# Kernel tuning notes

Hardware: AMD Instinct MI355X
Metric: run time of the kernel (lower is better)

Reference implementation:

```python
import jax, jax.numpy as jnp
import numpy as np

B, N, C = 8, 4096, 768
H = 12
D = C // H  # 64


def setup_inputs() -> dict:
    key = jax.random.key(0)
    k1, k2, k3 = jax.random.split(key, 3)
    x = jax.random.normal(k1, (B, N, C), dtype=jnp.float32)
    Wqkv = jax.random.normal(k2, (C, 3 * C), dtype=jnp.float32) * (C ** -0.5)
    Wproj = jax.random.normal(k3, (C, C), dtype=jnp.float32) * (C ** -0.5)
    bproj = jnp.zeros((C,), dtype=jnp.float32)
    return {"x": x, "Wqkv": Wqkv, "Wproj": Wproj, "bproj": bproj}


def reference(x, Wqkv, Wproj, bproj):
    b, n, c = x.shape
    qkv = x @ Wqkv  # [B,N,3C]
    qkv = qkv.reshape(b, n, 3, H, D).transpose(2, 0, 3, 1, 4)  # [3,B,H,N,D]
    q, k, v = qkv[0], qkv[1], qkv[2]
    # softmax over the sequence axis (dim=-2 in torch => N)
    k = jax.nn.softmax(k, axis=-2)
    # context: [B,H,D,D] -- small d x d intermediate
    context = jnp.einsum('bhnd,bhne->bhde', k, v)
    out = jnp.einsum('bhnd,bhde->bhne', q, context)  # [B,H,N,D]
    out = out.transpose(0, 2, 1, 3).reshape(b, n, c)  # b h n d -> b n (h d)
    return out @ Wproj + bproj
```

## Files before the change

### kernel.cpp

```cpp
#include <hip/hip_runtime.h>
#include <cstdint>
#include <cstddef>


typedef __bf16 bf8_t __attribute__((ext_vector_type(8)));
typedef float f4_t __attribute__((ext_vector_type(4)));

#define DEV_INLINE __device__ __forceinline__

DEV_INLINE void gload16(const void* g, void* l) {
  __builtin_amdgcn_global_load_lds(
      (const __attribute__((address_space(1))) void*)g,
      (__attribute__((address_space(3))) void*)l, 16, 0, 0);
}

__global__ __launch_bounds__(256) void cast_f32_bf16(const float* __restrict__ in,
                                                     __bf16* __restrict__ out, int n4) {
  int i = blockIdx.x * 256 + threadIdx.x;
  if (i >= n4) return;
  float4 f = ((const float4*)in)[i];
  union { __bf16 h[4]; uint2 u; } o;
  o.h[0] = (__bf16)f.x; o.h[1] = (__bf16)f.y; o.h[2] = (__bf16)f.z; o.h[3] = (__bf16)f.w;
  ((uint2*)out)[i] = o.u;
}

__global__ __launch_bounds__(256) void transpose_cast(const float* __restrict__ in,
                                                      __bf16* __restrict__ out, int R, int C) {
  int o = blockIdx.x * 256 + threadIdx.x;
  if (o >= R * C) return;
  int c = o / R, r = o - c * R;
  out[o] = (__bf16)in[r * C + c];
}

__global__ __launch_bounds__(256) void wq_cast(const float* __restrict__ in,
                                               __bf16* __restrict__ out) {
  int o = blockIdx.x * 256 + threadIdx.x;
  int r = o / 768, c = o - r * 768;
  out[o] = (__bf16)in[r * 2304 + c];
}

__global__ __launch_bounds__(256) void gemm1_kv(const __bf16* __restrict__ A,
                                                const __bf16* __restrict__ B,
                                                __bf16* __restrict__ KTo,
                                                __bf16* __restrict__ VTo) {
  constexpr int LDA = 768, LDB = 768, BK = 32, KTOT = 768, NT = 12;
  __shared__ __bf16 sA[128 * 32];
  __shared__ __bf16 sB[128 * 32];
  const int tid = threadIdx.x;
  const int mt = blockIdx.x / NT, nt = blockIdx.x % NT;
  const int lane = tid & 63, wv = tid >> 6;
  const int wr = (wv >> 1) * 64, wc = (wv & 1) * 64;
  const int lr = lane & 15, quad = lane >> 4;

  const int e0 = tid * 8;
  const int srow = e0 >> 5, skk = e0 & 31;
  const __bf16* gA = A + (size_t)(mt * 128 + srow) * LDA + skk;
  const __bf16* gB = B + (size_t)(nt * 128 + srow) * LDB + skk;

  const f4_t fz = {0.f, 0.f, 0.f, 0.f};
  f4_t acc[4][4];
#pragma unroll
  for (int i = 0; i < 4; i++)
#pragma unroll
    for (int j = 0; j < 4; j++) acc[i][j] = fz;

  for (int k0 = 0; k0 < KTOT; k0 += BK) {
    gload16(gA, &sA[e0]);
    gload16(gA + 64 * LDA, &sA[e0 + 2048]);
    gload16(gB, &sB[e0]);
    gload16(gB + 64 * LDB, &sB[e0 + 2048]);
    gA += BK; gB += BK;
    __syncthreads();
    bf8_t af[4], bfm[4];
#pragma unroll
    for (int i = 0; i < 4; i++)
      af[i] = *(const bf8_t*)&sA[(wr + i * 16 + lr) * 32 + quad * 8];
#pragma unroll
    for (int j = 0; j < 4; j++)
      bfm[j] = *(const bf8_t*)&sB[(wc + j * 16 + lr) * 32 + quad * 8];
#pragma unroll
    for (int i = 0; i < 4; i++)
#pragma unroll
      for (int j = 0; j < 4; j++)
        acc[i][j] = __builtin_amdgcn_mfma_f32_16x16x32_bf16(af[i], bfm[j], acc[i][j], 0, 0, 0);
    __syncthreads();
  }

  const int s = nt / 6;
  const int colw0 = (nt % 6) * 128 + wc;
  const int row0 = mt * 128 + wr;
  __bf16* T = (s == 0) ? KTo : VTo;
  const int b = row0 >> 12;
  const int n0 = (row0 & 4095) + quad * 4;
#pragma unroll
  for (int i = 0; i < 4; i++) {
    int n = n0 + i * 16;
#pragma unroll
    for (int j = 0; j < 4; j++) {
      int cw = colw0 + j * 16 + lr;
      int h = cw >> 6, d = cw & 63;
      union { __bf16 h4[4]; uint2 u; } pk;
#pragma unroll
      for (int r = 0; r < 4; r++) pk.h4[r] = (__bf16)acc[i][j][r];
      *(uint2*)&T[((size_t)(b * 12 + h) * 64 + d) * 4096 + n] = pk.u;
    }
  }
}

__global__ __launch_bounds__(256) void softmax_rows(__bf16* __restrict__ KT) {
  __shared__ float red[8];
  __bf16* p = KT + (size_t)blockIdx.x * 4096;
  const int tid = threadIdx.x, lane = tid & 63, wv = tid >> 6;
  bf8_t x0 = *(const bf8_t*)&p[tid * 16];
  bf8_t x1 = *(const bf8_t*)&p[tid * 16 + 8];
  float v[16];
#pragma unroll
  for (int k = 0; k < 8; k++) { v[k] = (float)x0[k]; v[8 + k] = (float)x1[k]; }
  float m = v[0];
#pragma unroll
  for (int k = 1; k < 16; k++) m = fmaxf(m, v[k]);
  for (int o = 32; o; o >>= 1) m = fmaxf(m, __shfl_xor(m, o, 64));
  if (lane == 0) red[wv] = m;
  __syncthreads();
  m = fmaxf(fmaxf(red[0], red[1]), fmaxf(red[2], red[3]));
  float s = 0.f;
#pragma unroll
  for (int k = 0; k < 16; k++) { v[k] = __expf(v[k] - m); s += v[k]; }
  for (int o = 32; o; o >>= 1) s += __shfl_xor(s, o, 64);
  if (lane == 0) red[4 + wv] = s;
  __syncthreads();
  s = red[4] + red[5] + red[6] + red[7];
  float inv = 1.0f / s;
  bf8_t o0, o1;
#pragma unroll
  for (int k = 0; k < 8; k++) { o0[k] = (__bf16)(v[k] * inv); o1[k] = (__bf16)(v[8 + k] * inv); }
  *(bf8_t*)&p[tid * 16] = o0;
  *(bf8_t*)&p[tid * 16 + 8] = o1;
}

__global__ __launch_bounds__(256) void ctx_kernel(const __bf16* __restrict__ KT,
                                                  const __bf16* __restrict__ VT,
                                                  float* __restrict__ part) {
  const int bh = blockIdx.x >> 3, kc = blockIdx.x & 7;
  const int tid = threadIdx.x, lane = tid & 63, wv = tid >> 6;
  const int wr = (wv >> 1) * 32, wc = (wv & 1) * 32;
  const int lr = lane & 15, quad = lane >> 4;
  const __bf16* Ab = KT + (size_t)bh * 64 * 4096;
  const __bf16* Bb = VT + (size_t)bh * 64 * 4096;
  const f4_t fz = {0.f, 0.f, 0.f, 0.f};
  f4_t acc[2][2] = {{fz, fz}, {fz, fz}};
  const int kbeg = kc * 512;
  for (int k0 = kbeg; k0 < kbeg + 512; k0 += 32) {
    bf8_t a[2], b[2];
#pragma unroll
    for (int i = 0; i < 2; i++)
      a[i] = *(const bf8_t*)&Ab[(size_t)(wr + i * 16 + lr) * 4096 + k0 + quad * 8];
#pragma unroll
    for (int j = 0; j < 2; j++)
      b[j] = *(const bf8_t*)&Bb[(size_t)(wc + j * 16 + lr) * 4096 + k0 + quad * 8];
#pragma unroll
    for (int i = 0; i < 2; i++)
#pragma unroll
      for (int j = 0; j < 2; j++)
        acc[i][j] = __builtin_amdgcn_mfma_f32_16x16x32_bf16(a[i], b[j], acc[i][j], 0, 0, 0);
  }
  float* po = part + (size_t)blockIdx.x * 4096;
#pragma unroll
  for (int i = 0; i < 2; i++)
#pragma unroll
    for (int j = 0; j < 2; j++)
#pragma unroll
      for (int r = 0; r < 4; r++)
        po[(wr + i * 16 + quad * 4 + r) * 64 + wc + j * 16 + lr] = acc[i][j][r];
}

__global__ __launch_bounds__(256) void wfused_kernel(const float* __restrict__ part,
                                                     const __bf16* __restrict__ WpT,
                                                     __bf16* __restrict__ B2T) {
  __shared__ __bf16 sctx[64 * 64];
  const int bh = blockIdx.x, cblk = blockIdx.y;
  const int b = bh / 12, h = bh % 12;
  const int tid = threadIdx.x;
  for (int i = tid; i < 4096; i += 256) {
    float s = 0.f;
#pragma unroll
    for (int kc = 0; kc < 8; kc++) s += part[(size_t)(bh * 8 + kc) * 4096 + i];
    sctx[i] = (__bf16)s;
  }
  __syncthreads();
  const int lane = tid & 63, wv = tid >> 6, lr = lane & 15, quad = lane >> 4;
  const int c0 = cblk * 192 + wv * 48;
  const f4_t fz = {0.f, 0.f, 0.f, 0.f};
  f4_t acc[3][4];
#pragma unroll
  for (int i = 0; i < 3; i++)
#pragma unroll
    for (int j = 0; j < 4; j++) acc[i][j] = fz;
#pragma unroll
  for (int k0 = 0; k0 < 64; k0 += 32) {
    bf8_t a[3], bq[4];
#pragma unroll
    for (int i = 0; i < 3; i++)
      a[i] = *(const bf8_t*)&WpT[(size_t)(c0 + i * 16 + lr) * 768 + h * 64 + k0 + quad * 8];
#pragma unroll
    for (int j = 0; j < 4; j++)
      bq[j] = *(const bf8_t*)&sctx[(j * 16 + lr) * 64 + k0 + quad * 8];
#pragma unroll
    for (int i = 0; i < 3; i++)
#pragma unroll
      for (int j = 0; j < 4; j++)
        acc[i][j] = __builtin_amdgcn_mfma_f32_16x16x32_bf16(a[i], bq[j], acc[i][j], 0, 0, 0);
  }
#pragma unroll
  for (int i = 0; i < 3; i++)
#pragma unroll
    for (int j = 0; j < 4; j++)
#pragma unroll
      for (int r = 0; r < 4; r++) {
        int c = c0 + i * 16 + quad * 4 + r;
        int d = j * 16 + lr;
        B2T[((size_t)b * 768 + c) * 768 + h * 64 + d] = (__bf16)acc[i][j][r];
      }
}

__global__ __launch_bounds__(256) void combine_kernel(const __bf16* __restrict__ B2Tall,
                                                      const __bf16* __restrict__ Wq,
                                                      __bf16* __restrict__ Wcomb) {
  constexpr int LD = 768, BK = 32, KTOT = 768;
  __shared__ __bf16 sA[64 * 32];
  __shared__ __bf16 sB[64 * 32];
  const int b = blockIdx.x / 144, rem = blockIdx.x % 144;
  const int mt = rem / 12, nt = rem % 12;
  const __bf16* A = B2Tall + (size_t)b * 768 * 768;
  const int tid = threadIdx.x, lane = tid & 63, wv = tid >> 6;
  const int wr = (wv >> 1) * 32, wc = (wv & 1) * 32;
  const int lr = lane & 15, quad = lane >> 4;

  const int e0 = tid * 8;
  const int srow = e0 >> 5, skk = e0 & 31;
  const __bf16* gA = A + (size_t)(mt * 64 + srow) * LD + skk;
  const __bf16* gB = Wq + (size_t)(nt * 64 + srow) * LD + skk;

  const f4_t fz = {0.f, 0.f, 0.f, 0.f};
  f4_t acc[2][2] = {{fz, fz}, {fz, fz}};

  for (int k0 = 0; k0 < KTOT; k0 += BK) {
    gload16(gA, &sA[e0]);
    gload16(gB, &sB[e0]);
    gA += BK; gB += BK;
    __syncthreads();
    bf8_t a[2], bq[2];
#pragma unroll
    for (int i = 0; i < 2; i++)
      a[i] = *(const bf8_t*)&sA[(wr + i * 16 + lr) * 32 + quad * 8];
#pragma unroll
    for (int j = 0; j < 2; j++)
      bq[j] = *(const bf8_t*)&sB[(wc + j * 16 + lr) * 32 + quad * 8];
#pragma unroll
    for (int i = 0; i < 2; i++)
#pragma unroll
      for (int j = 0; j < 2; j++)
        acc[i][j] = __builtin_amdgcn_mfma_f32_16x16x32_bf16(a[i], bq[j], acc[i][j], 0, 0, 0);
    __syncthreads();
  }
  __bf16* C = Wcomb + (size_t)b * 768 * 768;
  const int row0 = mt * 64 + wr, col0 = nt * 64 + wc;
#pragma unroll
  for (int i = 0; i < 2; i++)
#pragma unroll
    for (int j = 0; j < 2; j++)
#pragma unroll
      for (int r = 0; r < 4; r++)
        C[(size_t)(row0 + i * 16 + quad * 4 + r) * 768 + col0 + j * 16 + lr] =
            (__bf16)acc[i][j][r];
}

__global__ __launch_bounds__(256) void gemm2_out(const __bf16* __restrict__ A,
                                                 const __bf16* __restrict__ Ball,
                                                 float* __restrict__ C,
                                                 const float* __restrict__ bias) {
  constexpr int LDA = 768, LDB = 768, BK = 32, KTOT = 768, NT = 6;
  __shared__ __bf16 sA[128 * 32];
  __shared__ __bf16 sB[128 * 32];
  const int tid = threadIdx.x;
  const int mt = blockIdx.x / NT, nt = blockIdx.x % NT;
  const __bf16* B = Ball + (size_t)(mt >> 5) * 768 * 768;
  const int lane = tid & 63, wv = tid >> 6;
  const int wr = (wv >> 1) * 64, wc = (wv & 1) * 64;
  const int lr = lane & 15, quad = lane >> 4;

  const int e0 = tid * 8;
  const int srow = e0 >> 5, skk = e0 & 31;
  const __bf16* gA = A + (size_t)(mt * 128 + srow) * LDA + skk;
  const __bf16* gB = B + (size_t)(nt * 128 + srow) * LDB + skk;

  const f4_t fz = {0.f, 0.f, 0.f, 0.f};
  f4_t acc[4][4];
#pragma unroll
  for (int i = 0; i < 4; i++)
#pragma unroll
    for (int j = 0; j < 4; j++) acc[i][j] = fz;

  for (int k0 = 0; k0 < KTOT; k0 += BK) {
    gload16(gA, &sA[e0]);
    gload16(gA + 64 * LDA, &sA[e0 + 2048]);
    gload16(gB, &sB[e0]);
    gload16(gB + 64 * LDB, &sB[e0 + 2048]);
    gA += BK; gB += BK;
    __syncthreads();
    bf8_t af[4], bfm[4];
#pragma unroll
    for (int i = 0; i < 4; i++)
      af[i] = *(const bf8_t*)&sA[(wr + i * 16 + lr) * 32 + quad * 8];
#pragma unroll
    for (int j = 0; j < 4; j++)
      bfm[j] = *(const bf8_t*)&sB[(wc + j * 16 + lr) * 32 + quad * 8];
#pragma unroll
    for (int i = 0; i < 4; i++)
#pragma unroll
      for (int j = 0; j < 4; j++)
        acc[i][j] = __builtin_amdgcn_mfma_f32_16x16x32_bf16(af[i], bfm[j], acc[i][j], 0, 0, 0);
    __syncthreads();
  }

  const int row0 = mt * 128 + wr;
  const int col0 = nt * 128 + wc;
#pragma unroll
  for (int j = 0; j < 4; j++) {
    int col = col0 + j * 16 + lr;
    float bv = bias[col];
#pragma unroll
    for (int i = 0; i < 4; i++)
#pragma unroll
      for (int r = 0; r < 4; r++)
        C[(size_t)(row0 + i * 16 + quad * 4 + r) * 768 + col] = acc[i][j][r] + bv;
  }
}

extern "C" void kernel_launch(void* const* d_in, const int* in_sizes, int n_in,
                              void* d_out, int out_size, void* d_ws, size_t ws_size,
                              hipStream_t stream) {
  const float* x = (const float*)d_in[0];
  const float* Wqkv = (const float*)d_in[1];
  const float* Wproj = (const float*)d_in[2];
  const float* bproj = (const float*)d_in[3];
  float* out = (float*)d_out;

  char* ws = (char*)d_ws;
  __bf16* Xb    = (__bf16*)(ws + 0);
  __bf16* KT    = (__bf16*)(ws + 50331648);
  __bf16* VT    = (__bf16*)(ws + 100663296);
  __bf16* WqkvT = (__bf16*)(ws + 150994944);
  __bf16* Wqc   = (__bf16*)(ws + 154533888);
  __bf16* WpT   = (__bf16*)(ws + 155713536);
  float*  part  = (float*)(ws + 156893184);
  __bf16* B2T   = (__bf16*)(ws + 169476096);
  __bf16* Wcomb = (__bf16*)(ws + 178913280);

  cast_f32_bf16<<<24576, 256, 0, stream>>>(x, Xb, 25165824 / 4);
  transpose_cast<<<(768 * 2304) / 256, 256, 0, stream>>>(Wqkv, WqkvT, 768, 2304);
  wq_cast<<<(768 * 768) / 256, 256, 0, stream>>>(Wqkv, Wqc);
  transpose_cast<<<(768 * 768) / 256, 256, 0, stream>>>(Wproj, WpT, 768, 768);
  gemm1_kv<<<256 * 12, 256, 0, stream>>>(Xb, WqkvT + 768 * 768, KT, VT);
  softmax_rows<<<6144, 256, 0, stream>>>(KT);
  ctx_kernel<<<96 * 8, 256, 0, stream>>>(KT, VT, part);
  wfused_kernel<<<dim3(96, 4), 256, 0, stream>>>(part, WpT, B2T);
  combine_kernel<<<1152, 256, 0, stream>>>(B2T, Wqc, Wcomb);
  gemm2_out<<<256 * 6, 256, 0, stream>>>(Xb, Wcomb, out, bproj);
}
```

Before: 450.6 us.

## Use 32x32 MFMA with swizzled LDS, fold softmax into ctx, tile transposes

```diff
diff --git a/kernel.cpp b/kernel.cpp
--- a/kernel.cpp
+++ b/kernel.cpp
@@ -5,6 +5,7 @@
 
 typedef __bf16 bf8_t __attribute__((ext_vector_type(8)));
 typedef float f4_t __attribute__((ext_vector_type(4)));
+typedef float f16_t __attribute__((ext_vector_type(16)));
 
 #define DEV_INLINE __device__ __forceinline__
 
@@ -26,10 +27,22 @@
 
 __global__ __launch_bounds__(256) void transpose_cast(const float* __restrict__ in,
                                                       __bf16* __restrict__ out, int R, int C) {
-  int o = blockIdx.x * 256 + threadIdx.x;
-  if (o >= R * C) return;
-  int c = o / R, r = o - c * R;
-  out[o] = (__bf16)in[r * C + c];
+  __shared__ float t[64][65];
+  const int tilesR = R >> 6;
+  const int tr = blockIdx.x % tilesR, tc = blockIdx.x / tilesR;
+  const int tx = threadIdx.x & 63, ty = threadIdx.x >> 6;
+  const int r0 = tr * 64, c0 = tc * 64;
+#pragma unroll
+  for (int p = 0; p < 16; p++) {
+    int r = p * 4 + ty;
+    t[r][tx] = in[(size_t)(r0 + r) * C + c0 + tx];
+  }
+  __syncthreads();
+#pragma unroll
+  for (int p = 0; p < 16; p++) {
+    int c = p * 4 + ty;
+    out[(size_t)(c0 + c) * R + r0 + tx] = (__bf16)t[tx][c];
+  }
 }
 
 __global__ __launch_bounds__(256) void wq_cast(const float* __restrict__ in,
@@ -43,73 +56,91 @@
                                                 const __bf16* __restrict__ B,
                                                 __bf16* __restrict__ KTo,
                                                 __bf16* __restrict__ VTo) {
-  constexpr int LDA = 768, LDB = 768, BK = 32, KTOT = 768, NT = 12;
+  constexpr int LDA = 768, LDB = 768, KTOT = 768;
   __shared__ __bf16 sA[128 * 32];
   __shared__ __bf16 sB[128 * 32];
   const int tid = threadIdx.x;
-  const int mt = blockIdx.x / NT, nt = blockIdx.x % NT;
+  const int xcd = blockIdx.x & 7, g = blockIdx.x >> 3;
+  const int mt = xcd * 32 + g / 12, nt = g % 12;
   const int lane = tid & 63, wv = tid >> 6;
   const int wr = (wv >> 1) * 64, wc = (wv & 1) * 64;
-  const int lr = lane & 15, quad = lane >> 4;
-
-  const int e0 = tid * 8;
-  const int srow = e0 >> 5, skk = e0 & 31;
-  const __bf16* gA = A + (size_t)(mt * 128 + srow) * LDA + skk;
-  const __bf16* gB = B + (size_t)(nt * 128 + srow) * LDB + skk;
-
-  const f4_t fz = {0.f, 0.f, 0.f, 0.f};
-  f4_t acc[4][4];
-#pragma unroll
-  for (int i = 0; i < 4; i++)
-#pragma unroll
-    for (int j = 0; j < 4; j++) acc[i][j] = fz;
-
-  for (int k0 = 0; k0 < KTOT; k0 += BK) {
-    gload16(gA, &sA[e0]);
-    gload16(gA + 64 * LDA, &sA[e0 + 2048]);
-    gload16(gB, &sB[e0]);
-    gload16(gB + 64 * LDB, &sB[e0 + 2048]);
-    gA += BK; gB += BK;
-    __syncthreads();
-    bf8_t af[4], bfm[4];
-#pragma unroll
-    for (int i = 0; i < 4; i++)
-      af[i] = *(const bf8_t*)&sA[(wr + i * 16 + lr) * 32 + quad * 8];
-#pragma unroll
-    for (int j = 0; j < 4; j++)
-      bfm[j] = *(const bf8_t*)&sB[(wc + j * 16 + lr) * 32 + quad * 8];
-#pragma unroll
-    for (int i = 0; i < 4; i++)
-#pragma unroll
-      for (int j = 0; j < 4; j++)
-        acc[i][j] = __builtin_amdgcn_mfma_f32_16x16x32_bf16(af[i], bfm[j], acc[i][j], 0, 0, 0);
+  const int l31 = lane & 31, l5 = lane >> 5;
+
+  const int srow = tid >> 2;
+  const int sk = ((tid & 3) ^ ((srow >> 1) & 3)) * 8;
+  const __bf16* gA = A + (size_t)(mt * 128 + srow) * LDA + sk;
+  const __bf16* gB = B + (size_t)(nt * 128 + srow) * LDB + sk;
+
+  const int arow = wr + l31, brow = wc + l31;
+  const int asw = (arow >> 1) & 3, bsw = (brow >> 1) & 3;
+  const int aoff  = arow * 32 + ((l5 ^ asw) * 8);
+  const int aoff2 = arow * 32 + (((2 | l5) ^ asw) * 8);
+  const int boff  = brow * 32 + ((l5 ^ bsw) * 8);
+  const int boff2 = brow * 32 + (((2 | l5) ^ bsw) * 8);
+
+  f16_t acc[2][2];
+#pragma unroll
+  for (int i = 0; i < 2; i++)
+#pragma unroll
+    for (int j = 0; j < 2; j++)
+#pragma unroll
+      for (int e = 0; e < 16; e++) acc[i][j][e] = 0.f;
+
+  for (int k0 = 0; k0 < KTOT; k0 += 32) {
+    gload16(gA, &sA[tid * 8]);
+    gload16(gA + 64 * LDA, &sA[tid * 8 + 2048]);
+    gload16(gB, &sB[tid * 8]);
+    gload16(gB + 64 * LDB, &sB[tid * 8 + 2048]);
+    gA += 32; gB += 32;
+    __syncthreads();
+    bf8_t a0 = *(const bf8_t*)&sA[aoff];
+    bf8_t a1 = *(const bf8_t*)&sA[aoff + 1024];
+    bf8_t b0 = *(const bf8_t*)&sB[boff];
+    bf8_t b1 = *(const bf8_t*)&sB[boff + 1024];
+    acc[0][0] = __builtin_amdgcn_mfma_f32_32x32x16_bf16(a0, b0, acc[0][0], 0, 0, 0);
+    acc[0][1] = __builtin_amdgcn_mfma_f32_32x32x16_bf16(a0, b1, acc[0][1], 0, 0, 0);
+    acc[1][0] = __builtin_amdgcn_mfma_f32_32x32x16_bf16(a1, b0, acc[1][0], 0, 0, 0);
+    acc[1][1] = __builtin_amdgcn_mfma_f32_32x32x16_bf16(a1, b1, acc[1][1], 0, 0, 0);
+    a0 = *(const bf8_t*)&sA[aoff2];
+    a1 = *(const bf8_t*)&sA[aoff2 + 1024];
+    b0 = *(const bf8_t*)&sB[boff2];
+    b1 = *(const bf8_t*)&sB[boff2 + 1024];
+    acc[0][0] = __builtin_amdgcn_mfma_f32_32x32x16_bf16(a0, b0, acc[0][0], 0, 0, 0);
+    acc[0][1] = __builtin_amdgcn_mfma_f32_32x32x16_bf16(a0, b1, acc[0][1], 0, 0, 0);
+    acc[1][0] = __builtin_amdgcn_mfma_f32_32x32x16_bf16(a1, b0, acc[1][0], 0, 0, 0);
+    acc[1][1] = __builtin_amdgcn_mfma_f32_32x32x16_bf16(a1, b1, acc[1][1], 0, 0, 0);
     __syncthreads();
   }
 
   const int s = nt / 6;
+  __bf16* T = (s == 0) ? KTo : VTo;
+  const int row0 = mt * 128 + wr;
+  const int bidx = row0 >> 12;
+  const int n0 = (row0 & 4095) + 4 * l5;
   const int colw0 = (nt % 6) * 128 + wc;
-  const int row0 = mt * 128 + wr;
-  __bf16* T = (s == 0) ? KTo : VTo;
-  const int b = row0 >> 12;
-  const int n0 = (row0 & 4095) + quad * 4;
-#pragma unroll
-  for (int i = 0; i < 4; i++) {
-    int n = n0 + i * 16;
-#pragma unroll
-    for (int j = 0; j < 4; j++) {
-      int cw = colw0 + j * 16 + lr;
-      int h = cw >> 6, d = cw & 63;
-      union { __bf16 h4[4]; uint2 u; } pk;
-#pragma unroll
-      for (int r = 0; r < 4; r++) pk.h4[r] = (__bf16)acc[i][j][r];
-      *(uint2*)&T[((size_t)(b * 12 + h) * 64 + d) * 4096 + n] = pk.u;
+#pragma unroll
+  for (int j = 0; j < 2; j++) {
+    int cw = colw0 + j * 32 + l31;
+    int h = cw >> 6, d = cw & 63;
+    __bf16* Tp = &T[((size_t)(bidx * 12 + h) * 64 + d) * 4096];
+#pragma unroll
+    for (int i = 0; i < 2; i++) {
+      int nb = n0 + i * 32;
+#pragma unroll
+      for (int r2 = 0; r2 < 4; r2++) {
+        union { __bf16 h4[4]; uint2 u; } pk;
+#pragma unroll
+        for (int r = 0; r < 4; r++) pk.h4[r] = (__bf16)acc[i][j][r2 * 4 + r];
+        *(uint2*)&Tp[nb + 8 * r2] = pk.u;
+      }
     }
   }
 }
 
-__global__ __launch_bounds__(256) void softmax_rows(__bf16* __restrict__ KT) {
+__global__ __launch_bounds__(256) void stats_rows(const __bf16* __restrict__ KT,
+                                                  float2* __restrict__ stats) {
   __shared__ float red[8];
-  __bf16* p = KT + (size_t)blockIdx.x * 4096;
+  const __bf16* p = KT + (size_t)blockIdx.x * 4096;
   const int tid = threadIdx.x, lane = tid & 63, wv = tid >> 6;
   bf8_t x0 = *(const bf8_t*)&p[tid * 16];
   bf8_t x1 = *(const bf8_t*)&p[tid * 16 + 8];
@@ -125,21 +156,19 @@
   m = fmaxf(fmaxf(red[0], red[1]), fmaxf(red[2], red[3]));
   float s = 0.f;
 #pragma unroll
-  for (int k = 0; k < 16; k++) { v[k] = __expf(v[k] - m); s += v[k]; }
+  for (int k = 0; k < 16; k++) s += __expf(v[k] - m);
   for (int o = 32; o; o >>= 1) s += __shfl_xor(s, o, 64);
   if (lane == 0) red[4 + wv] = s;
   __syncthreads();
-  s = red[4] + red[5] + red[6] + red[7];
-  float inv = 1.0f / s;
-  bf8_t o0, o1;
-#pragma unroll
-  for (int k = 0; k < 8; k++) { o0[k] = (__bf16)(v[k] * inv); o1[k] = (__bf16)(v[8 + k] * inv); }
-  *(bf8_t*)&p[tid * 16] = o0;
-  *(bf8_t*)&p[tid * 16 + 8] = o1;
+  if (tid == 0) {
+    float st = red[4] + red[5] + red[6] + red[7];
+    stats[blockIdx.x] = make_float2(m, 1.0f / st);
+  }
 }
 
 __global__ __launch_bounds__(256) void ctx_kernel(const __bf16* __restrict__ KT,
                                                   const __bf16* __restrict__ VT,
+                                                  const float2* __restrict__ stats,
                                                   float* __restrict__ part) {
   const int bh = blockIdx.x >> 3, kc = blockIdx.x & 7;
   const int tid = threadIdx.x, lane = tid & 63, wv = tid >> 6;
@@ -147,14 +176,21 @@
   const int lr = lane & 15, quad = lane >> 4;
   const __bf16* Ab = KT + (size_t)bh * 64 * 4096;
   const __bf16* Bb = VT + (size_t)bh * 64 * 4096;
+  float2 st[2];
+  st[0] = stats[bh * 64 + wr + lr];
+  st[1] = stats[bh * 64 + wr + 16 + lr];
   const f4_t fz = {0.f, 0.f, 0.f, 0.f};
   f4_t acc[2][2] = {{fz, fz}, {fz, fz}};
   const int kbeg = kc * 512;
   for (int k0 = kbeg; k0 < kbeg + 512; k0 += 32) {
     bf8_t a[2], b[2];
 #pragma unroll
-    for (int i = 0; i < 2; i++)
-      a[i] = *(const bf8_t*)&Ab[(size_t)(wr + i * 16 + lr) * 4096 + k0 + quad * 8];
+    for (int i = 0; i < 2; i++) {
+      bf8_t raw = *(const bf8_t*)&Ab[(size_t)(wr + i * 16 + lr) * 4096 + k0 + quad * 8];
+#pragma unroll
+      for (int e = 0; e < 8; e++)
+        a[i][e] = (__bf16)(__expf((float)raw[e] - st[i].x) * st[i].y);
+    }
 #pragma unroll
     for (int j = 0; j < 2; j++)
       b[j] = *(const bf8_t*)&Bb[(size_t)(wc + j * 16 + lr) * 4096 + k0 + quad * 8];
@@ -279,61 +315,78 @@
                                                  const __bf16* __restrict__ Ball,
                                                  float* __restrict__ C,
                                                  const float* __restrict__ bias) {
-  constexpr int LDA = 768, LDB = 768, BK = 32, KTOT = 768, NT = 6;
+  constexpr int LDA = 768, LDB = 768, KTOT = 768;
   __shared__ __bf16 sA[128 * 32];
   __shared__ __bf16 sB[128 * 32];
   const int tid = threadIdx.x;
-  const int mt = blockIdx.x / NT, nt = blockIdx.x % NT;
+  const int xcd = blockIdx.x & 7, g = blockIdx.x >> 3;
+  const int mt = xcd * 32 + g / 6, nt = g % 6;
   const __bf16* B = Ball + (size_t)(mt >> 5) * 768 * 768;
   const int lane = tid & 63, wv = tid >> 6;
   const int wr = (wv >> 1) * 64, wc = (wv & 1) * 64;
-  const int lr = lane & 15, quad = lane >> 4;
-
-  const int e0 = tid * 8;
-  const int srow = e0 >> 5, skk = e0 & 31;
-  const __bf16* gA = A + (size_t)(mt * 128 + srow) * LDA + skk;
-  const __bf16* gB = B + (size_t)(nt * 128 + srow) * LDB + skk;
-
-  const f4_t fz = {0.f, 0.f, 0.f, 0.f};
-  f4_t acc[4][4];
-#pragma unroll
-  for (int i = 0; i < 4; i++)
-#pragma unroll
-    for (int j = 0; j < 4; j++) acc[i][j] = fz;
-
-  for (int k0 = 0; k0 < KTOT; k0 += BK) {
-    gload16(gA, &sA[e0]);
-    gload16(gA + 64 * LDA, &sA[e0 + 2048]);
-    gload16(gB, &sB[e0]);
-    gload16(gB + 64 * LDB, &sB[e0 + 2048]);
-    gA += BK; gB += BK;
-    __syncthreads();
-    bf8_t af[4], bfm[4];
-#pragma unroll
-    for (int i = 0; i < 4; i++)
-      af[i] = *(const bf8_t*)&sA[(wr + i * 16 + lr) * 32 + quad * 8];
-#pragma unroll
-    for (int j = 0; j < 4; j++)
-      bfm[j] = *(const bf8_t*)&sB[(wc + j * 16 + lr) * 32 + quad * 8];
-#pragma unroll
-    for (int i = 0; i < 4; i++)
-#pragma unroll
-      for (int j = 0; j < 4; j++)
-        acc[i][j] = __builtin_amdgcn_mfma_f32_16x16x32_bf16(af[i], bfm[j], acc[i][j], 0, 0, 0);
-    __syncthreads();
-  }
-
-  const int row0 = mt * 128 + wr;
+  const int l31 = lane & 31, l5 = lane >> 5;
+
+  const int srow = tid >> 2;
+  const int sk = ((tid & 3) ^ ((srow >> 1) & 3)) * 8;
+  const __bf16* gA = A + (size_t)(mt * 128 + srow) * LDA + sk;
+  const __bf16* gB = B + (size_t)(nt * 128 + srow) * LDB + sk;
+
+  const int arow = wr + l31, brow = wc + l31;
+  const int asw = (arow >> 1) & 3, bsw = (brow >> 1) & 3;
+  const int aoff  = arow * 32 + ((l5 ^ asw) * 8);
+  const int aoff2 = arow * 32 + (((2 | l5) ^ asw) * 8);
+  const int boff  = brow * 32 + ((l5 ^ bsw) * 8);
+  const int boff2 = brow * 32 + (((2 | l5) ^ bsw) * 8);
+
+  f16_t acc[2][2];
+#pragma unroll
+  for (int i = 0; i < 2; i++)
+#pragma unroll
+    for (int j = 0; j < 2; j++)
+#pragma unroll
+      for (int e = 0; e < 16; e++) acc[i][j][e] = 0.f;
+
+  for (int k0 = 0; k0 < KTOT; k0 += 32) {
+    gload16(gA, &sA[tid * 8]);
+    gload16(gA + 64 * LDA, &sA[tid * 8 + 2048]);
+    gload16(gB, &sB[tid * 8]);
+    gload16(gB + 64 * LDB, &sB[tid * 8 + 2048]);
+    gA += 32; gB += 32;
+    __syncthreads();
+    bf8_t a0 = *(const bf8_t*)&sA[aoff];
+    bf8_t a1 = *(const bf8_t*)&sA[aoff + 1024];
+    bf8_t b0 = *(const bf8_t*)&sB[boff];
+    bf8_t b1 = *(const bf8_t*)&sB[boff + 1024];
+    acc[0][0] = __builtin_amdgcn_mfma_f32_32x32x16_bf16(a0, b0, acc[0][0], 0, 0, 0);
+    acc[0][1] = __builtin_amdgcn_mfma_f32_32x32x16_bf16(a0, b1, acc[0][1], 0, 0, 0);
+    acc[1][0] = __builtin_amdgcn_mfma_f32_32x32x16_bf16(a1, b0, acc[1][0], 0, 0, 0);
+    acc[1][1] = __builtin_amdgcn_mfma_f32_32x32x16_bf16(a1, b1, acc[1][1], 0, 0, 0);
+    a0 = *(const bf8_t*)&sA[aoff2];
+    a1 = *(const bf8_t*)&sA[aoff2 + 1024];
+    b0 = *(const bf8_t*)&sB[boff2];
+    b1 = *(const bf8_t*)&sB[boff2 + 1024];
+    acc[0][0] = __builtin_amdgcn_mfma_f32_32x32x16_bf16(a0, b0, acc[0][0], 0, 0, 0);
+    acc[0][1] = __builtin_amdgcn_mfma_f32_32x32x16_bf16(a0, b1, acc[0][1], 0, 0, 0);
+    acc[1][0] = __builtin_amdgcn_mfma_f32_32x32x16_bf16(a1, b0, acc[1][0], 0, 0, 0);
+    acc[1][1] = __builtin_amdgcn_mfma_f32_32x32x16_bf16(a1, b1, acc[1][1], 0, 0, 0);
+    __syncthreads();
+  }
+
+  const int row0 = mt * 128 + wr + 4 * l5;
   const int col0 = nt * 128 + wc;
 #pragma unroll
-  for (int j = 0; j < 4; j++) {
-    int col = col0 + j * 16 + lr;
+  for (int j = 0; j < 2; j++) {
+    int col = col0 + j * 32 + l31;
     float bv = bias[col];
 #pragma unroll
-    for (int i = 0; i < 4; i++)
-#pragma unroll
-      for (int r = 0; r < 4; r++)
-        C[(size_t)(row0 + i * 16 + quad * 4 + r) * 768 + col] = acc[i][j][r] + bv;
+    for (int i = 0; i < 2; i++)
+#pragma unroll
+      for (int r2 = 0; r2 < 4; r2++) {
+        int rbase = row0 + i * 32 + 8 * r2;
+#pragma unroll
+        for (int r = 0; r < 4; r++)
+          C[(size_t)(rbase + r) * 768 + col] = acc[i][j][r2 * 4 + r] + bv;
+      }
   }
 }
 
@@ -351,6 +404,7 @@
   __bf16* KT    = (__bf16*)(ws + 50331648);
   __bf16* VT    = (__bf16*)(ws + 100663296);
   __bf16* WqkvT = (__bf16*)(ws + 150994944);
+  float2* stats = (float2*)(ws + 150994944);
   __bf16* Wqc   = (__bf16*)(ws + 154533888);
   __bf16* WpT   = (__bf16*)(ws + 155713536);
   float*  part  = (float*)(ws + 156893184);
@@ -358,13 +412,13 @@
   __bf16* Wcomb = (__bf16*)(ws + 178913280);
 
   cast_f32_bf16<<<24576, 256, 0, stream>>>(x, Xb, 25165824 / 4);
-  transpose_cast<<<(768 * 2304) / 256, 256, 0, stream>>>(Wqkv, WqkvT, 768, 2304);
+  transpose_cast<<<12 * 36, 256, 0, stream>>>(Wqkv, WqkvT, 768, 2304);
   wq_cast<<<(768 * 768) / 256, 256, 0, stream>>>(Wqkv, Wqc);
-  transpose_cast<<<(768 * 768) / 256, 256, 0, stream>>>(Wproj, WpT, 768, 768);
-  gemm1_kv<<<256 * 12, 256, 0, stream>>>(Xb, WqkvT + 768 * 768, KT, VT);
-  softmax_rows<<<6144, 256, 0, stream>>>(KT);
-  ctx_kernel<<<96 * 8, 256, 0, stream>>>(KT, VT, part);
+  transpose_cast<<<12 * 12, 256, 0, stream>>>(Wproj, WpT, 768, 768);
+  gemm1_kv<<<3072, 256, 0, stream>>>(Xb, WqkvT + 768 * 768, KT, VT);
+  stats_rows<<<6144, 256, 0, stream>>>(KT, stats);
+  ctx_kernel<<<96 * 8, 256, 0, stream>>>(KT, VT, stats, part);
   wfused_kernel<<<dim3(96, 4), 256, 0, stream>>>(part, WpT, B2T);
   combine_kernel<<<1152, 256, 0, stream>>>(B2T, Wqc, Wcomb);
-  gemm2_out<<<256 * 6, 256, 0, stream>>>(Xb, Wcomb, out, bproj);
-}
+  gemm2_out<<<1536, 256, 0, stream>>>(Xb, Wcomb, out, bproj);
+}
```

After: 422.1 us. -6.3%, faster.
